# Kernel tuning notes

Hardware: AMD Instinct MI355X
Metric: run time of the kernel (lower is better)

Reference implementation:

```python
import jax, jax.numpy as jnp
import numpy as np

D = 768          # model dim (ViT-Base)
H = 12           # num heads
DH = 64          # head dim
DFF = 4 * D      # mlp hidden
SMAX = 1024      # max sequence length in the packed batch
LENS = np.array([1024, 896, 768, 640, 512, 448, 256, 64], dtype=np.int32)
TOTAL = int(LENS.sum())  # 4608
LN_EPS = 1e-6
NEG = -1e30


def _ln(x, w, b):
    mu = jnp.mean(x, axis=-1, keepdims=True)
    var = jnp.mean(jnp.square(x - mu), axis=-1, keepdims=True)
    return (x - mu) * jax.lax.rsqrt(var + LN_EPS) * w + b


def setup_inputs() -> dict:
    key = jax.random.key(0)
    ks = jax.random.split(key, 16)
    s = 0.02
    cu = jnp.asarray(np.concatenate([[0], np.cumsum(LENS)]).astype(np.int32))
    return {
        "x": jax.random.normal(ks[0], (TOTAL, D), jnp.float32),
        "norm1_w": jnp.ones((D,), jnp.float32),
        "norm1_b": jnp.zeros((D,), jnp.float32),
        "qkv_w": jax.random.normal(ks[1], (3 * D, D), jnp.float32) * s,
        "qkv_b": jnp.zeros((3 * D,), jnp.float32),
        "proj_w": jax.random.normal(ks[2], (D, D), jnp.float32) * s,
        "proj_b": jnp.zeros((D,), jnp.float32),
        "ls1_gamma": jax.random.normal(ks[3], (D,), jnp.float32) * 0.1,
        "norm2_w": jnp.ones((D,), jnp.float32),
        "norm2_b": jnp.zeros((D,), jnp.float32),
        "fc1_w": jax.random.normal(ks[4], (DFF, D), jnp.float32) * s,
        "fc1_b": jnp.zeros((DFF,), jnp.float32),
        "fc2_w": jax.random.normal(ks[5], (D, DFF), jnp.float32) * s,
        "fc2_b": jnp.zeros((D,), jnp.float32),
        "ls2_gamma": jax.random.normal(ks[6], (D,), jnp.float32) * 0.1,
        "cu_seqlens": cu,
    }


def reference(x, norm1_w, norm1_b, qkv_w, qkv_b, proj_w, proj_b, ls1_gamma,
              norm2_w, norm2_b, fc1_w, fc1_b, fc2_w, fc2_b, ls2_gamma,
              cu_seqlens):
    total = x.shape[0]
    B = cu_seqlens.shape[0] - 1
    tok = jnp.arange(total)
    seg = jnp.searchsorted(cu_seqlens[1:], tok, side="right")  # [Total]
    pos = tok - cu_seqlens[seg]                                 # [Total]
    lens = cu_seqlens[1:] - cu_seqlens[:-1]                     # [B]

    # --- attention branch ---
    xn = _ln(x, norm1_w, norm1_b)
    qkv = (xn @ qkv_w.T + qkv_b).reshape(total, 3, H, DH)
    q, k, v = qkv[:, 0], qkv[:, 1], qkv[:, 2]                   # [Total,H,DH]

    # pad packed ragged tokens to [B, SMAX, H, DH]
    def pad(t):
        return jnp.zeros((B, SMAX, H, DH), t.dtype).at[seg, pos].set(t)
    qp, kp, vp = pad(q), pad(k), pad(v)

    valid = jnp.arange(SMAX)[None, :] < lens[:, None]           # [B,SMAX]
    scores = jnp.einsum("bqhd,bkhd->bhqk", qp, kp) * (DH ** -0.5)
    scores = jnp.where(valid[:, None, None, :], scores, NEG)
    attn = jax.nn.softmax(scores, axis=-1)
    out = jnp.einsum("bhqk,bkhd->bqhd", attn, vp)
    out = out[seg, pos].reshape(total, D)                       # back to packed

    attn_out = out @ proj_w.T + proj_b
    x = x + ls1_gamma * attn_out

    # --- mlp branch ---
    xn2 = _ln(x, norm2_w, norm2_b)
    h = jax.nn.gelu(xn2 @ fc1_w.T + fc1_b, approximate=False)
    h = h @ fc2_w.T + fc2_b
    return x + ls2_gamma * h
```

## Files before the change

kernel.cpp:

```cpp
#include <hip/hip_runtime.h>
#include <hip/hip_bf16.h>
#include <stdint.h>

#define D 768
#define HEADS 12
#define DHEAD 64
#define DFF 3072
#define TOTAL 4608
#define NSEG 8

typedef __bf16 bf16;
typedef __bf16 bf16x8 __attribute__((ext_vector_type(8)));
typedef __bf16 bf16x4 __attribute__((ext_vector_type(4)));
typedef float f32x4 __attribute__((ext_vector_type(4)));

__device__ __forceinline__ void gld_lds16(const void* g, void* l) {
  __builtin_amdgcn_global_load_lds(
      (const __attribute__((address_space(1))) void*)g,
      (__attribute__((address_space(3))) void*)(uintptr_t)l, 16, 0, 0);
}

__device__ __forceinline__ void lds_barrier() {
  asm volatile("s_waitcnt lgkmcnt(0)\n\ts_barrier" ::: "memory");
}

__global__ __launch_bounds__(256) void cvt_all_kernel(
    const float* __restrict__ a, const float* __restrict__ b,
    const float* __restrict__ c, const float* __restrict__ d,
    bf16* __restrict__ out, int nA, int nAB, int nABC, int nTot) {
  int i = blockIdx.x * blockDim.x + threadIdx.x;
  if (i >= nTot) return;
  const float* src;
  int j;
  if (i < nA) { src = a; j = i; }
  else if (i < nAB) { src = b; j = i - nA; }
  else if (i < nABC) { src = c; j = i - nAB; }
  else { src = d; j = i - nABC; }
  float4 v = ((const float4*)src)[j];
  bf16x4 o;
  o[0] = (bf16)v.x; o[1] = (bf16)v.y; o[2] = (bf16)v.z; o[3] = (bf16)v.w;
  ((bf16x4*)out)[i] = o;
}

__global__ __launch_bounds__(256) void ln_kernel(
    const float* __restrict__ x, const float* __restrict__ w,
    const float* __restrict__ b, bf16* __restrict__ out) {
  __shared__ float red[8];
  int row = blockIdx.x;
  const float* xr = x + (size_t)row * D;
  int t = threadIdx.x;
  float v[3];
  float s = 0.f, s2 = 0.f;
#pragma unroll
  for (int j = 0; j < 3; j++) {
    v[j] = xr[t + 256 * j];
    s += v[j]; s2 += v[j] * v[j];
  }
#pragma unroll
  for (int m = 1; m <= 32; m <<= 1) {
    s += __shfl_xor(s, m);
    s2 += __shfl_xor(s2, m);
  }
  int wave = t >> 6, lane = t & 63;
  if (lane == 0) { red[wave] = s; red[4 + wave] = s2; }
  __syncthreads();
  s = red[0] + red[1] + red[2] + red[3];
  s2 = red[4] + red[5] + red[6] + red[7];
  float mu = s * (1.f / 768.f);
  float var = s2 * (1.f / 768.f) - mu * mu;
  float rstd = rsqrtf(var + 1e-6f);
#pragma unroll
  for (int j = 0; j < 3; j++) {
    int c = t + 256 * j;
    out[(size_t)row * D + c] = (bf16)((v[j] - mu) * rstd * w[c] + b[c]);
  }
}

__device__ __forceinline__ float fast_gelu(float v) {
  float u = v * (0.7978845608f + 0.0356774081f * v * v);
  float e = exp2f(2.8853900818f * u);
  float th = 1.f - 2.f * __builtin_amdgcn_rcpf(1.f + e);
  return 0.5f * v * (1.f + th);
}

template <int MODE, int TN, int BK, int GX, int GY>
__global__ __launch_bounds__(256) void gemm_kernel(
    const bf16* __restrict__ A, const bf16* __restrict__ W,
    const float* __restrict__ bias, const float* __restrict__ res,
    const float* __restrict__ gamma, bf16* __restrict__ outb,
    float* __restrict__ outf, int N, int K) {
  constexpr int NJ = TN / 32;
  constexpr int KH = BK / 32;
  constexpr int CG = BK / 8;
  constexpr int SH = (BK == 32) ? 1 : 0;
  constexpr int LPR = BK / 8;
  constexpr int RS = 64 / LPR;
  constexpr int RB = TN / 4;
  __shared__ __align__(16) bf16 As[2][128 * BK];
  __shared__ __align__(16) bf16 Bs[2][TN * BK];

  const int g = blockIdx.x;
  const int xc = g & 7, q = g >> 3;
  const int bx = q % GX, by = xc + 8 * (q / GX);
  if (by >= GY) return;
  const int m0 = by * 128, n0 = bx * TN;

  const int t = threadIdx.x, wave = t >> 6, lane = t & 63;
  const int quad = lane >> 4, l16 = lane & 15;
  const int wm = (wave & 1) * 64, wn = (wave >> 1) * (TN / 2);

  const int ar = lane / LPR, ac = lane % LPR;
  const int acg = ac ^ (((wave * 32 + ar) >> SH) & (CG - 1));
  const int bcg = ac ^ (((wave * RB + ar) >> SH) & (CG - 1));
  const bf16* gA = A + (size_t)(m0 + wave * 32 + ar) * K + acg * 8;
  const bf16* gB = W + (size_t)(n0 + wave * RB + ar) * K + bcg * 8;

  auto stage = [&](int buf) {
#pragma unroll
    for (int n = 0; n < 32 / RS; n++)
      gld_lds16(gA + (size_t)n * RS * K, &As[buf][(wave * 32 + n * RS) * BK]);
#pragma unroll
    for (int n = 0; n < RB / RS; n++)
      gld_lds16(gB + (size_t)n * RS * K, &Bs[buf][(wave * RB + n * RS) * BK]);
    gA += BK; gB += BK;
  };

  stage(0);

  f32x4 acc[4][NJ] = {};
  int cur = 0;
  for (int k0 = 0; k0 < K; k0 += BK) {
    __syncthreads();
    if (k0 + BK < K) stage(cur ^ 1);
    const bf16* as = As[cur];
    const bf16* bs = Bs[cur];
    bf16x8 af[KH][4], bg[KH][NJ];
#pragma unroll
    for (int kh = 0; kh < KH; kh++) {
#pragma unroll
      for (int i = 0; i < 4; i++) {
        int R = wm + i * 16 + l16;
        af[kh][i] = *(const bf16x8*)&as[R * BK + 8 * ((kh * 4 + quad) ^ ((R >> SH) & (CG - 1)))];
      }
#pragma unroll
      for (int j = 0; j < NJ; j++) {
        int R = wn + j * 16 + l16;
        bg[kh][j] = *(const bf16x8*)&bs[R * BK + 8 * ((kh * 4 + quad) ^ ((R >> SH) & (CG - 1)))];
      }
    }
#pragma unroll
    for (int kh = 0; kh < KH; kh++)
#pragma unroll
      for (int i = 0; i < 4; i++)
#pragma unroll
        for (int j = 0; j < NJ; j++)
          acc[i][j] = __builtin_amdgcn_mfma_f32_16x16x32_bf16(af[kh][i], bg[kh][j], acc[i][j], 0, 0, 0);
    cur ^= 1;
  }

#pragma unroll
  for (int i = 0; i < 4; i++)
#pragma unroll
    for (int j = 0; j < NJ; j++)
#pragma unroll
      for (int r = 0; r < 4; r++) {
        int row = m0 + wm + i * 16 + quad * 4 + r;
        int col = n0 + wn + j * 16 + l16;
        float v = acc[i][j][r] + bias[col];
        if (MODE == 0) {
          outb[(size_t)row * N + col] = (bf16)v;
        } else if (MODE == 1) {
          outf[(size_t)row * N + col] = res[(size_t)row * N + col] + gamma[col] * v;
        } else {
          outb[(size_t)row * N + col] = (bf16)fast_gelu(v);
        }
      }
}

__global__ __launch_bounds__(256) void attn_kernel(
    const bf16* __restrict__ qkv, const int* __restrict__ cu,
    bf16* __restrict__ attn) {
  __shared__ __align__(16) bf16 Ks[2][64][72];
  __shared__ __align__(16) bf16 VTs[2][64][64];

  const int qt = blockIdx.y, h = blockIdx.x;
  const int tok0 = qt * 64;
  int b = 0;
  while (cu[b + 1] <= tok0) b++;
  const int s0 = cu[b], S = cu[b + 1] - s0;
  const int n = S >> 6;

  const int t = threadIdx.x, wave = t >> 6, lane = t & 63;
  const int quad = lane >> 4, l16 = lane & 15;

  const size_t qrow = (size_t)(tok0 + wave * 16 + l16) * (3 * D) + h * 64;
  const bf16x8 bq0 = *(const bf16x8*)&qkv[qrow + quad * 8];
  const bf16x8 bq1 = *(const bf16x8*)&qkv[qrow + 32 + quad * 8];

  const int srow = t >> 2, sc0 = (t & 3) * 16;
  const size_t kbase = (size_t)(s0 + srow) * (3 * D) + h * 64 + sc0 + D;
  const int vr0 = (t & 15) * 4, vd0 = (t >> 4) * 4;
  const size_t vbase = (size_t)(s0 + vr0) * (3 * D) + h * 64 + vd0 + 2 * D;
  const int kB0 = ((vr0 >> 5) << 5) | (((vr0 >> 2) & 3) << 3) | (((vr0 >> 4) & 1) << 2);

  f32x4 Oacc[4] = {};
  float li = 0.f;
  const float SC = 0.125f * 1.44269504089f;

  bf16x8 kA0, kA1, kB0r, kB1r;
  bf16x4 vA[4], vB[4];

  auto loadT = [&](int tile, bf16x8& k0, bf16x8& k1, bf16x4* vp) {
    const size_t ko = kbase + (size_t)tile * 64 * (3 * D);
    const size_t vo = vbase + (size_t)tile * 64 * (3 * D);
    k0 = *(const bf16x8*)&qkv[ko];
    k1 = *(const bf16x8*)&qkv[ko + 8];
#pragma unroll
    for (int i = 0; i < 4; i++)
      vp[i] = *(const bf16x4*)&qkv[vo + (size_t)i * (3 * D)];
  };
  auto writeT = [&](int buf, const bf16x8& k0, const bf16x8& k1, const bf16x4* vp) {
    *(bf16x8*)&Ks[buf][srow][sc0] = k0;
    *(bf16x8*)&Ks[buf][srow][sc0 + 8] = k1;
#pragma unroll
    for (int j = 0; j < 4; j++) {
      int d = vd0 + j;
      bf16x4 w;
      w[0] = vp[0][j]; w[1] = vp[1][j]; w[2] = vp[2][j]; w[3] = vp[3][j];
      *(bf16x4*)&VTs[buf][d][kB0 ^ ((d & 7) * 8)] = w;
    }
  };
  auto computeT = [&](int buf) {
    f32x4 sac[4];
#pragma unroll
    for (int nt = 0; nt < 4; nt++) {
      bf16x8 ak0 = *(const bf16x8*)&Ks[buf][nt * 16 + l16][quad * 8];
      bf16x8 ak1 = *(const bf16x8*)&Ks[buf][nt * 16 + l16][32 + quad * 8];
      f32x4 z = {};
      z = __builtin_amdgcn_mfma_f32_16x16x32_bf16(ak0, bq0, z, 0, 0, 0);
      sac[nt] = __builtin_amdgcn_mfma_f32_16x16x32_bf16(ak1, bq1, z, 0, 0, 0);
    }
    bf16x8 pv0, pv1;
    float ls = 0.f;
#pragma unroll
    for (int r = 0; r < 4; r++) {
      float e0 = exp2f(sac[0][r] * SC);
      float e1 = exp2f(sac[1][r] * SC);
      float e2 = exp2f(sac[2][r] * SC);
      float e3 = exp2f(sac[3][r] * SC);
      ls += (e0 + e1) + (e2 + e3);
      pv0[r] = (bf16)e0; pv0[4 + r] = (bf16)e1;
      pv1[r] = (bf16)e2; pv1[4 + r] = (bf16)e3;
    }
    li += ls;
    const int vsw = (l16 & 7) * 8;
#pragma unroll
    for (int dt = 0; dt < 4; dt++) {
      bf16x8 av0 = *(const bf16x8*)&VTs[buf][dt * 16 + l16][(quad * 8) ^ vsw];
      bf16x8 av1 = *(const bf16x8*)&VTs[buf][dt * 16 + l16][(32 + quad * 8) ^ vsw];
      Oacc[dt] = __builtin_amdgcn_mfma_f32_16x16x32_bf16(av0, pv0, Oacc[dt], 0, 0, 0);
      Oacc[dt] = __builtin_amdgcn_mfma_f32_16x16x32_bf16(av1, pv1, Oacc[dt], 0, 0, 0);
    }
  };

  loadT(0, kA0, kA1, vA);
  if (n > 1) loadT(1, kB0r, kB1r, vB);
  writeT(0, kA0, kA1, vA);

  for (int tt = 0; tt < n; tt += 2) {
    lds_barrier();
    if (tt + 1 < n) writeT(1, kB0r, kB1r, vB);
    if (tt + 2 < n) loadT(tt + 2, kA0, kA1, vA);
    computeT(0);
    if (tt + 1 >= n) break;
    lds_barrier();
    if (tt + 2 < n) writeT(0, kA0, kA1, vA);
    if (tt + 3 < n) loadT(tt + 3, kB0r, kB1r, vB);
    computeT(1);
  }

  li += __shfl_xor(li, 16);
  li += __shfl_xor(li, 32);
  const float inv = 1.f / li;

  __syncthreads();
  bf16(*Osh)[72] = (bf16(*)[72])Ks[0];
  const int orow = wave * 16 + l16;
#pragma unroll
  for (int dt = 0; dt < 4; dt++) {
    int dg = dt * 16 + quad * 4;
    bf16x4 w;
#pragma unroll
    for (int r = 0; r < 4; r++) w[r] = (bf16)(Oacc[dt][r] * inv);
    *(bf16x4*)&Osh[orow][dg ^ ((l16 & 7) * 8)] = w;
  }
  const int osw = (l16 & 7) * 8;
  bf16x8 o0 = *(const bf16x8*)&Osh[orow][(quad * 16) ^ osw];
  bf16x8 o1 = *(const bf16x8*)&Osh[orow][(quad * 16 + 8) ^ osw];
  const size_t obase = (size_t)(tok0 + orow) * D + h * 64 + quad * 16;
  *(bf16x8*)&attn[obase] = o0;
  *(bf16x8*)&attn[obase + 8] = o1;
}

extern "C" void kernel_launch(void* const* d_in, const int* in_sizes, int n_in,
                              void* d_out, int out_size, void* d_ws,
                              size_t ws_size, hipStream_t stream) {
  const float* x       = (const float*)d_in[0];
  const float* norm1_w = (const float*)d_in[1];
  const float* norm1_b = (const float*)d_in[2];
  const float* qkv_w   = (const float*)d_in[3];
  const float* qkv_b   = (const float*)d_in[4];
  const float* proj_w  = (const float*)d_in[5];
  const float* proj_b  = (const float*)d_in[6];
  const float* ls1     = (const float*)d_in[7];
  const float* norm2_w = (const float*)d_in[8];
  const float* norm2_b = (const float*)d_in[9];
  const float* fc1_w   = (const float*)d_in[10];
  const float* fc1_b   = (const float*)d_in[11];
  const float* fc2_w   = (const float*)d_in[12];
  const float* fc2_b   = (const float*)d_in[13];
  const float* ls2     = (const float*)d_in[14];
  const int*   cu      = (const int*)d_in[15];
  float* out = (float*)d_out;

  char* ws = (char*)d_ws;
  size_t off = 0;
  auto alloc = [&](size_t bytes) {
    void* p = ws + off;
    off += (bytes + 255) & ~(size_t)255;
    return p;
  };
  bf16* w_qkv  = (bf16*)alloc((size_t)3 * D * D * 2);
  bf16* w_proj = (bf16*)alloc((size_t)D * D * 2);
  bf16* w_fc1  = (bf16*)alloc((size_t)DFF * D * 2);
  bf16* w_fc2  = (bf16*)alloc((size_t)D * DFF * 2);
  bf16* xn     = (bf16*)alloc((size_t)TOTAL * D * 2);
  bf16* qkv    = (bf16*)alloc((size_t)TOTAL * 3 * D * 2);
  bf16* attnb  = (bf16*)alloc((size_t)TOTAL * D * 2);
  float* x1    = (float*)alloc((size_t)TOTAL * D * 4);
  bf16* hbuf   = qkv;

  {
    int nA   = 3 * D * D / 4;
    int nAB  = nA + D * D / 4;
    int nABC = nAB + DFF * D / 4;
    int nTot = nABC + D * DFF / 4;
    cvt_all_kernel<<<(nTot + 255) / 256, 256, 0, stream>>>(
        qkv_w, proj_w, fc1_w, fc2_w, w_qkv, nA, nAB, nABC, nTot);
  }

  ln_kernel<<<TOTAL, 256, 0, stream>>>(x, norm1_w, norm1_b, xn);

  constexpr int GY = TOTAL / 128;
  constexpr int GYP = ((GY + 7) / 8) * 8;

  gemm_kernel<0, 128, 64, 18, GY><<<18 * GYP, 256, 0, stream>>>(
      xn, w_qkv, qkv_b, nullptr, nullptr, qkv, nullptr, 3 * D, D);

  dim3 ga(HEADS, TOTAL / 64);
  attn_kernel<<<ga, 256, 0, stream>>>(qkv, cu, attnb);

  gemm_kernel<1, 64, 64, 12, GY><<<12 * GYP, 256, 0, stream>>>(
      attnb, w_proj, proj_b, x, ls1, nullptr, x1, D, D);

  ln_kernel<<<TOTAL, 256, 0, stream>>>(x1, norm2_w, norm2_b, xn);

  gemm_kernel<2, 128, 64, 24, GY><<<24 * GYP, 256, 0, stream>>>(
      xn, w_fc1, fc1_b, nullptr, nullptr, hbuf, nullptr, DFF, D);

  gemm_kernel<1, 64, 64, 12, GY><<<12 * GYP, 256, 0, stream>>>(
      hbuf, w_fc2, fc2_b, x1, ls2, nullptr, out, D, DFF);
}
```

Measured before the change: 260.1 us.

## Process two query tiles per attention block and refine GEMM pipeline waits

The attention kernel now assigns two 64-row query tiles from the same segment to each block, so every K/V tile staged in LDS is reused by both. This halves K/V global loads and LDS staging per query. The grid becomes 37 by 12 blocks, computed from the segment lengths. The GEMM loop replaces __syncthreads with explicit vmcnt-based waits so the next stage's async loads can overlap the barrier. The cost is more registers, possible lower occupancy, and the grid size 37 is hardcoded to these sequence lengths.

Measured after the change: 262.4 us. No clear change (+0.9%).

```diff
diff --git a/kernel.cpp b/kernel.cpp
--- a/kernel.cpp
+++ b/kernel.cpp
@@ -96,6 +96,7 @@
   constexpr int LPR = BK / 8;
   constexpr int RS = 64 / LPR;
   constexpr int RB = TN / 4;
+  constexpr int NSTG = 32 / RS + RB / RS;
   __shared__ __align__(16) bf16 As[2][128 * BK];
   __shared__ __align__(16) bf16 Bs[2][TN * BK];
 
@@ -130,8 +131,16 @@
   f32x4 acc[4][NJ] = {};
   int cur = 0;
   for (int k0 = 0; k0 < K; k0 += BK) {
-    __syncthreads();
-    if (k0 + BK < K) stage(cur ^ 1);
+    if (k0 + BK < K) {
+      asm volatile("s_waitcnt lgkmcnt(0)\n\ts_barrier" ::: "memory");
+      stage(cur ^ 1);
+      if constexpr (NSTG == 8)
+        asm volatile("s_waitcnt vmcnt(8)\n\ts_barrier" ::: "memory");
+      else
+        asm volatile("s_waitcnt vmcnt(6)\n\ts_barrier" ::: "memory");
+    } else {
+      asm volatile("s_waitcnt vmcnt(0)\n\ts_barrier" ::: "memory");
+    }
     const bf16* as = As[cur];
     const bf16* bs = Bs[cur];
     bf16x8 af[KH][4], bg[KH][NJ];
@@ -183,19 +192,30 @@
   __shared__ __align__(16) bf16 Ks[2][64][72];
   __shared__ __align__(16) bf16 VTs[2][64][64];
 
-  const int qt = blockIdx.y, h = blockIdx.x;
-  const int tok0 = qt * 64;
-  int b = 0;
-  while (cu[b + 1] <= tok0) b++;
-  const int s0 = cu[b], S = cu[b + 1] - s0;
-  const int n = S >> 6;
+  const int h = blockIdx.y;
+  int j = blockIdx.x, s0 = 0, n = 0, m = 0;
+  for (int s = 0; s < NSEG; s++) {
+    int beg = cu[s], ns = (cu[s + 1] - beg) >> 6;
+    int ms = (ns + 1) >> 1;
+    if (j < ms) { s0 = beg; n = ns; m = ms; break; }
+    j -= ms;
+  }
+  const int tokA = s0 + j * 64;
+  const bool hasB = (j + m) < n;
+  const int tokB = s0 + (j + m) * 64;
 
   const int t = threadIdx.x, wave = t >> 6, lane = t & 63;
   const int quad = lane >> 4, l16 = lane & 15;
 
-  const size_t qrow = (size_t)(tok0 + wave * 16 + l16) * (3 * D) + h * 64;
-  const bf16x8 bq0 = *(const bf16x8*)&qkv[qrow + quad * 8];
-  const bf16x8 bq1 = *(const bf16x8*)&qkv[qrow + 32 + quad * 8];
+  const size_t qrowA = (size_t)(tokA + wave * 16 + l16) * (3 * D) + h * 64;
+  const bf16x8 bqA0 = *(const bf16x8*)&qkv[qrowA + quad * 8];
+  const bf16x8 bqA1 = *(const bf16x8*)&qkv[qrowA + 32 + quad * 8];
+  bf16x8 bqB0 = {}, bqB1 = {};
+  if (hasB) {
+    const size_t qrowB = (size_t)(tokB + wave * 16 + l16) * (3 * D) + h * 64;
+    bqB0 = *(const bf16x8*)&qkv[qrowB + quad * 8];
+    bqB1 = *(const bf16x8*)&qkv[qrowB + 32 + quad * 8];
+  }
 
   const int srow = t >> 2, sc0 = (t & 3) * 16;
   const size_t kbase = (size_t)(s0 + srow) * (3 * D) + h * 64 + sc0 + D;
@@ -203,8 +223,8 @@
   const size_t vbase = (size_t)(s0 + vr0) * (3 * D) + h * 64 + vd0 + 2 * D;
   const int kB0 = ((vr0 >> 5) << 5) | (((vr0 >> 2) & 3) << 3) | (((vr0 >> 4) & 1) << 2);
 
-  f32x4 Oacc[4] = {};
-  float li = 0.f;
+  f32x4 OA[4] = {}, OB[4] = {};
+  float liA = 0.f, liB = 0.f;
   const float SC = 0.125f * 1.44269504089f;
 
   bf16x8 kA0, kA1, kB0r, kB1r;
@@ -223,43 +243,57 @@
     *(bf16x8*)&Ks[buf][srow][sc0] = k0;
     *(bf16x8*)&Ks[buf][srow][sc0 + 8] = k1;
 #pragma unroll
-    for (int j = 0; j < 4; j++) {
-      int d = vd0 + j;
+    for (int jj = 0; jj < 4; jj++) {
+      int d = vd0 + jj;
       bf16x4 w;
-      w[0] = vp[0][j]; w[1] = vp[1][j]; w[2] = vp[2][j]; w[3] = vp[3][j];
+      w[0] = vp[0][jj]; w[1] = vp[1][jj]; w[2] = vp[2][jj]; w[3] = vp[3][jj];
       *(bf16x4*)&VTs[buf][d][kB0 ^ ((d & 7) * 8)] = w;
     }
   };
   auto computeT = [&](int buf) {
-    f32x4 sac[4];
+    f32x4 sacA[4], sacB[4];
 #pragma unroll
     for (int nt = 0; nt < 4; nt++) {
       bf16x8 ak0 = *(const bf16x8*)&Ks[buf][nt * 16 + l16][quad * 8];
       bf16x8 ak1 = *(const bf16x8*)&Ks[buf][nt * 16 + l16][32 + quad * 8];
-      f32x4 z = {};
-      z = __builtin_amdgcn_mfma_f32_16x16x32_bf16(ak0, bq0, z, 0, 0, 0);
-      sac[nt] = __builtin_amdgcn_mfma_f32_16x16x32_bf16(ak1, bq1, z, 0, 0, 0);
-    }
-    bf16x8 pv0, pv1;
-    float ls = 0.f;
+      f32x4 zA = {};
+      zA = __builtin_amdgcn_mfma_f32_16x16x32_bf16(ak0, bqA0, zA, 0, 0, 0);
+      sacA[nt] = __builtin_amdgcn_mfma_f32_16x16x32_bf16(ak1, bqA1, zA, 0, 0, 0);
+      if (hasB) {
+        f32x4 zB = {};
+        zB = __builtin_amdgcn_mfma_f32_16x16x32_bf16(ak0, bqB0, zB, 0, 0, 0);
+        sacB[nt] = __builtin_amdgcn_mfma_f32_16x16x32_bf16(ak1, bqB1, zB, 0, 0, 0);
+      }
+    }
+    bf16x8 pA0, pA1, pB0, pB1;
+    float lsA = 0.f, lsB = 0.f;
 #pragma unroll
     for (int r = 0; r < 4; r++) {
-      float e0 = exp2f(sac[0][r] * SC);
-      float e1 = exp2f(sac[1][r] * SC);
-      float e2 = exp2f(sac[2][r] * SC);
-      float e3 = exp2f(sac[3][r] * SC);
-      ls += (e0 + e1) + (e2 + e3);
-      pv0[r] = (bf16)e0; pv0[4 + r] = (bf16)e1;
-      pv1[r] = (bf16)e2; pv1[4 + r] = (bf16)e3;
-    }
-    li += ls;
+      float e0 = exp2f(sacA[0][r] * SC), e1 = exp2f(sacA[1][r] * SC);
+      float e2 = exp2f(sacA[2][r] * SC), e3 = exp2f(sacA[3][r] * SC);
+      lsA += (e0 + e1) + (e2 + e3);
+      pA0[r] = (bf16)e0; pA0[4 + r] = (bf16)e1;
+      pA1[r] = (bf16)e2; pA1[4 + r] = (bf16)e3;
+      if (hasB) {
+        float f0 = exp2f(sacB[0][r] * SC), f1 = exp2f(sacB[1][r] * SC);
+        float f2 = exp2f(sacB[2][r] * SC), f3 = exp2f(sacB[3][r] * SC);
+        lsB += (f0 + f1) + (f2 + f3);
+        pB0[r] = (bf16)f0; pB0[4 + r] = (bf16)f1;
+        pB1[r] = (bf16)f2; pB1[4 + r] = (bf16)f3;
+      }
+    }
+    liA += lsA; liB += lsB;
     const int vsw = (l16 & 7) * 8;
 #pragma unroll
     for (int dt = 0; dt < 4; dt++) {
       bf16x8 av0 = *(const bf16x8*)&VTs[buf][dt * 16 + l16][(quad * 8) ^ vsw];
       bf16x8 av1 = *(const bf16x8*)&VTs[buf][dt * 16 + l16][(32 + quad * 8) ^ vsw];
-      Oacc[dt] = __builtin_amdgcn_mfma_f32_16x16x32_bf16(av0, pv0, Oacc[dt], 0, 0, 0);
-      Oacc[dt] = __builtin_amdgcn_mfma_f32_16x16x32_bf16(av1, pv1, Oacc[dt], 0, 0, 0);
+      OA[dt] = __builtin_amdgcn_mfma_f32_16x16x32_bf16(av0, pA0, OA[dt], 0, 0, 0);
+      OA[dt] = __builtin_amdgcn_mfma_f32_16x16x32_bf16(av1, pA1, OA[dt], 0, 0, 0);
+      if (hasB) {
+        OB[dt] = __builtin_amdgcn_mfma_f32_16x16x32_bf16(av0, pB0, OB[dt], 0, 0, 0);
+        OB[dt] = __builtin_amdgcn_mfma_f32_16x16x32_bf16(av1, pB1, OB[dt], 0, 0, 0);
+      }
     }
   };
 
@@ -279,27 +313,46 @@
     computeT(1);
   }
 
-  li += __shfl_xor(li, 16);
-  li += __shfl_xor(li, 32);
-  const float inv = 1.f / li;
+  liA += __shfl_xor(liA, 16); liA += __shfl_xor(liA, 32);
+  liB += __shfl_xor(liB, 16); liB += __shfl_xor(liB, 32);
+  const float invA = 1.f / liA;
+  const float invB = hasB ? 1.f / liB : 0.f;
 
   __syncthreads();
-  bf16(*Osh)[72] = (bf16(*)[72])Ks[0];
   const int orow = wave * 16 + l16;
-#pragma unroll
-  for (int dt = 0; dt < 4; dt++) {
-    int dg = dt * 16 + quad * 4;
-    bf16x4 w;
-#pragma unroll
-    for (int r = 0; r < 4; r++) w[r] = (bf16)(Oacc[dt][r] * inv);
-    *(bf16x4*)&Osh[orow][dg ^ ((l16 & 7) * 8)] = w;
-  }
   const int osw = (l16 & 7) * 8;
-  bf16x8 o0 = *(const bf16x8*)&Osh[orow][(quad * 16) ^ osw];
-  bf16x8 o1 = *(const bf16x8*)&Osh[orow][(quad * 16 + 8) ^ osw];
-  const size_t obase = (size_t)(tok0 + orow) * D + h * 64 + quad * 16;
-  *(bf16x8*)&attn[obase] = o0;
-  *(bf16x8*)&attn[obase + 8] = o1;
+  {
+    bf16(*Osh)[72] = (bf16(*)[72])Ks[0];
+#pragma unroll
+    for (int dt = 0; dt < 4; dt++) {
+      int dg = dt * 16 + quad * 4;
+      bf16x4 w;
+#pragma unroll
+      for (int r = 0; r < 4; r++) w[r] = (bf16)(OA[dt][r] * invA);
+      *(bf16x4*)&Osh[orow][dg ^ osw] = w;
+    }
+    bf16x8 o0 = *(const bf16x8*)&Osh[orow][(quad * 16) ^ osw];
+    bf16x8 o1 = *(const bf16x8*)&Osh[orow][(quad * 16 + 8) ^ osw];
+    const size_t ob = (size_t)(tokA + orow) * D + h * 64 + quad * 16;
+    *(bf16x8*)&attn[ob] = o0;
+    *(bf16x8*)&attn[ob + 8] = o1;
+  }
+  if (hasB) {
+    bf16(*Osh)[72] = (bf16(*)[72])Ks[1];
+#pragma unroll
+    for (int dt = 0; dt < 4; dt++) {
+      int dg = dt * 16 + quad * 4;
+      bf16x4 w;
+#pragma unroll
+      for (int r = 0; r < 4; r++) w[r] = (bf16)(OB[dt][r] * invB);
+      *(bf16x4*)&Osh[orow][dg ^ osw] = w;
+    }
+    bf16x8 o0 = *(const bf16x8*)&Osh[orow][(quad * 16) ^ osw];
+    bf16x8 o1 = *(const bf16x8*)&Osh[orow][(quad * 16 + 8) ^ osw];
+    const size_t ob = (size_t)(tokB + orow) * D + h * 64 + quad * 16;
+    *(bf16x8*)&attn[ob] = o0;
+    *(bf16x8*)&attn[ob + 8] = o1;
+  }
 }
 
 extern "C" void kernel_launch(void* const* d_in, const int* in_sizes, int n_in,
@@ -357,7 +410,7 @@
   gemm_kernel<0, 128, 64, 18, GY><<<18 * GYP, 256, 0, stream>>>(
       xn, w_qkv, qkv_b, nullptr, nullptr, qkv, nullptr, 3 * D, D);
 
-  dim3 ga(HEADS, TOTAL / 64);
+  dim3 ga(37, HEADS);
   attn_kernel<<<ga, 256, 0, stream>>>(qkv, cu, attnb);
 
   gemm_kernel<1, 64, 64, 12, GY><<<12 * GYP, 256, 0, stream>>>(
```
